# Optimization experiments

Measured on AMD Instinct MI355X. Metric: run time of the kernel, lower is better.

## Reference

```python
import jax, jax.numpy as jnp
import numpy as np

N, E = 50000, 400000
IN_CH, HID, HEADS, EDGE_DIM = 128, 64, 4, 3
NEG_SLOPE = 0.2


def gatv2_conv(x, src, dst, edge_attr, Wl, Wr, We, att, bias):
    # x: [N, F_in]; Wl/Wr: [H*C, F_in]; We: [H*C, edge_dim]; att: [H, C]; bias: [C]
    H, C = att.shape
    n = x.shape[0]
    xl = (x @ Wl.T).reshape(n, H, C)   # source-side transform (lin_l)
    xr = (x @ Wr.T).reshape(n, H, C)   # target-side transform (lin_r)
    e = (edge_attr @ We.T).reshape(-1, H, C)
    z = jax.nn.leaky_relu(xl[src] + xr[dst] + e, NEG_SLOPE)  # [E,H,C]
    alpha = jnp.einsum('ehc,hc->eh', z, att)                 # [E,H]
    # segment softmax over incoming edges per destination node
    amax = jax.ops.segment_max(alpha, dst, num_segments=n)
    alpha = jnp.exp(alpha - amax[dst])
    denom = jax.ops.segment_sum(alpha, dst, num_segments=n)
    alpha = alpha / (denom[dst] + 1e-16)
    msg = xl[src] * alpha[:, :, None]                        # [E,H,C]
    out = jax.ops.segment_sum(msg, dst, num_segments=n)      # [N,H,C]
    return out.mean(axis=1) + bias                           # concat=False -> head mean


def setup_inputs() -> dict:
    key = jax.random.key(0)
    ks = jax.random.split(key, 16)
    s = 0.1
    return {
        'x': jax.random.normal(ks[0], (N, IN_CH), jnp.float32),
        'edge_index': jax.random.randint(ks[1], (2, E), 0, N, jnp.int32),
        'edge_attr': jax.random.normal(ks[2], (E, EDGE_DIM), jnp.float32),
        'Wl1': jax.random.normal(ks[3], (HEADS * HID, IN_CH), jnp.float32) * s,
        'Wr1': jax.random.normal(ks[4], (HEADS * HID, IN_CH), jnp.float32) * s,
        'We1': jax.random.normal(ks[5], (HEADS * HID, EDGE_DIM), jnp.float32) * s,
        'att1': jax.random.normal(ks[6], (HEADS, HID), jnp.float32) * s,
        'b1': jnp.zeros((HID,), jnp.float32),
        'Wl2': jax.random.normal(ks[7], (HEADS * HID, HID), jnp.float32) * s,
        'Wr2': jax.random.normal(ks[8], (HEADS * HID, HID), jnp.float32) * s,
        'We2': jax.random.normal(ks[9], (HEADS * HID, EDGE_DIM), jnp.float32) * s,
        'att2': jax.random.normal(ks[10], (HEADS, HID), jnp.float32) * s,
        'b2': jnp.zeros((HID,), jnp.float32),
        'prelu_w': jnp.full((HID,), 0.25, jnp.float32),
    }


def reference(x, edge_index, edge_attr, Wl1, Wr1, We1, att1, b1, Wl2, Wr2, We2, att2, b2, prelu_w):
    src, dst = edge_index[0], edge_index[1]
    h = gatv2_conv(x, src, dst, edge_attr, Wl1, Wr1, We1, att1, b1)
    h = gatv2_conv(h, src, dst, edge_attr, Wl2, Wr2, We2, att2, b2)
    return jnp.where(h >= 0, h, prelu_w * h)  # PReLU, per-channel weight
```

## Files before the change

### kernel.cpp

```cpp
#include <hip/hip_runtime.h>
#include <hip/hip_bf16.h>

#define HC 256

typedef __attribute__((ext_vector_type(8))) short bf16x8;
typedef __attribute__((ext_vector_type(4))) float f32x4;
typedef __attribute__((ext_vector_type(2))) float f32x2;

__device__ __forceinline__ void gl_lds16(const void* g, void* l) {
  __builtin_amdgcn_global_load_lds(
      (const __attribute__((address_space(1))) unsigned int*)g,
      (__attribute__((address_space(3))) unsigned int*)l, 16, 0, 0);
}

__device__ __forceinline__ void cast_w_one(const float* Wl, const float* Wr,
                                           ushort* WT, int F, int idx) {
  int col = idx / F, f = idx - col * F;
  float v = (col < 256) ? Wl[col * F + f] : Wr[(col - 256) * F + f];
  __hip_bfloat16 h = __float2bfloat16(v);
  WT[(size_t)col * F + f] = *(ushort*)&h;
}

__global__ void k_weights_hist(const float* __restrict__ Wl1, const float* __restrict__ Wr1,
                               ushort* __restrict__ WT1, const float* __restrict__ Wl2,
                               const float* __restrict__ Wr2, ushort* __restrict__ WT2,
                               const int* __restrict__ ei, int* __restrict__ deg, int E_) {
  int idx = blockIdx.x * blockDim.x + threadIdx.x;
  const int t1 = 512 * 128, t2 = 512 * 64;
  if (idx < t1) {
    cast_w_one(Wl1, Wr1, WT1, 128, idx);
  } else if (idx < t1 + t2) {
    cast_w_one(Wl2, Wr2, WT2, 64, idx - t1);
  } else {
    int e = idx - t1 - t2;
    if (e < E_) atomicAdd(&deg[ei[E_ + e]], 1);
  }
}

template <int F>
__global__ __launch_bounds__(256) void gemm_mfma(const ushort* __restrict__ A,
                                                 const ushort* __restrict__ WT,
                                                 ushort* __restrict__ xlb,
                                                 ushort* __restrict__ xrb, int n_nodes) {
  constexpr int NSTEP = F / 64;
  __shared__ __align__(16) ushort As[128 * 64];
  __shared__ __align__(16) ushort Bs[128 * 64];
  const int tid = threadIdx.x;
  const int wv = tid >> 6, lane = tid & 63;
  const int m16 = lane & 15, quad = lane >> 4;
  const int col0 = blockIdx.x * 128;
  const int row0 = blockIdx.y * 128;
  const int wm = (wv >> 1) * 64, wn = (wv & 1) * 64;

  f32x4 acc[4][4];
#pragma unroll
  for (int i = 0; i < 4; ++i)
#pragma unroll
    for (int j = 0; j < 4; ++j) acc[i][j] = (f32x4){0.f, 0.f, 0.f, 0.f};

#pragma unroll
  for (int s = 0; s < NSTEP; ++s) {
    const int khat = s * 64;
    __syncthreads();
#pragma unroll
    for (int t = 0; t < 4; ++t) {
      const int sl16 = tid + 256 * t;
      const int row = sl16 >> 3, sl = sl16 & 7;
      const int gch = sl ^ (row & 7);
      const int grow = row0 + row;
      if (grow < n_nodes)
        gl_lds16(A + (size_t)grow * F + khat + gch * 8, As + sl16 * 8);
      gl_lds16(WT + (size_t)(col0 + row) * F + khat + gch * 8, Bs + sl16 * 8);
    }
    __syncthreads();
#pragma unroll
    for (int kh = 0; kh < 2; ++kh) {
      bf16x8 af[4], bf[4];
#pragma unroll
      for (int i = 0; i < 4; ++i) {
        const int row = wm + i * 16 + m16;
        const int slot = (kh * 4 + quad) ^ (row & 7);
        af[i] = *(bf16x8*)&As[row * 64 + slot * 8];
      }
#pragma unroll
      for (int j = 0; j < 4; ++j) {
        const int col = wn + j * 16 + m16;
        const int slot = (kh * 4 + quad) ^ (col & 7);
        bf[j] = *(bf16x8*)&Bs[col * 64 + slot * 8];
      }
#pragma unroll
      for (int i = 0; i < 4; ++i)
#pragma unroll
        for (int j = 0; j < 4; ++j)
          acc[i][j] =
              __builtin_amdgcn_mfma_f32_16x16x32_bf16(af[i], bf[j], acc[i][j], 0, 0, 0);
    }
  }
  const bool is_xl = (col0 < 256);
#pragma unroll
  for (int i = 0; i < 4; ++i) {
#pragma unroll
    for (int r = 0; r < 4; ++r) {
      const int grow = row0 + wm + i * 16 + quad * 4 + r;
      if (grow < n_nodes) {
#pragma unroll
        for (int j = 0; j < 4; ++j) {
          const float v = acc[i][j][r];
          const int col = col0 + wn + j * 16 + m16;
          __hip_bfloat16 h = __float2bfloat16(v);
          if (is_xl)
            xlb[(size_t)grow * 256 + col] = *(ushort*)&h;
          else
            xrb[(size_t)grow * 256 + (col - 256)] = *(ushort*)&h;
        }
      }
    }
  }
}

__global__ void k_scan_local(const int* __restrict__ deg, int* __restrict__ rowstart,
                             int* __restrict__ partial, int n) {
  __shared__ int a[256], b[256];
  const int t = threadIdx.x;
  const int i = blockIdx.x * 256 + t;
  const int v = (i < n) ? deg[i] : 0;
  a[t] = v;
  __syncthreads();
  int* cur = a;
  int* nxt = b;
  for (int off = 1; off < 256; off <<= 1) {
    int x = cur[t];
    if (t >= off) x += cur[t - off];
    nxt[t] = x;
    __syncthreads();
    int* tmp = cur; cur = nxt; nxt = tmp;
  }
  const int incl = cur[t];
  if (i < n) rowstart[i] = incl - v;
  if (t == 255) partial[blockIdx.x] = incl;
}

__global__ void k_scan_partial(int* __restrict__ partial, int nblk,
                               int* __restrict__ ssrc, float4* __restrict__ sea, int E_) {
  __shared__ int a[256], b[256];
  const int t = threadIdx.x;
  if (t < 8) {
    ssrc[E_ + t] = 0;
    sea[E_ + t] = make_float4(0.f, 0.f, 0.f, 0.f);
  }
  const int v = (t < nblk) ? partial[t] : 0;
  a[t] = v;
  __syncthreads();
  int* cur = a;
  int* nxt = b;
  for (int off = 1; off < 256; off <<= 1) {
    int x = cur[t];
    if (t >= off) x += cur[t - off];
    nxt[t] = x;
    __syncthreads();
    int* tmp = cur; cur = nxt; nxt = tmp;
  }
  if (t < nblk) partial[t] = cur[t] - v;
}

__global__ void k_add_off(int* __restrict__ rowstart, int* __restrict__ cursor,
                          const int* __restrict__ partial, int n, int E_) {
  int i = blockIdx.x * blockDim.x + threadIdx.x;
  if (i < n) {
    int v = rowstart[i] + partial[i >> 8];
    rowstart[i] = v;
    cursor[i] = v;
  }
  if (i == 0) rowstart[n] = E_;
}

__global__ void k_prep(const float* __restrict__ x, ushort* __restrict__ A,
                       const int* __restrict__ ei, const float* __restrict__ ea,
                       int* __restrict__ cursor, int* __restrict__ ssrc,
                       float4* __restrict__ sea, int n, int E_) {
  const int nx8 = n * 16;
  int idx = blockIdx.x * blockDim.x + threadIdx.x;
  if (idx < nx8) {
    const float4* xp = (const float4*)x + (size_t)idx * 2;
    float4 v0 = xp[0], v1 = xp[1];
    float vv[8] = {v0.x, v0.y, v0.z, v0.w, v1.x, v1.y, v1.z, v1.w};
    __align__(16) ushort hb[8];
#pragma unroll
    for (int j = 0; j < 8; ++j) {
      __hip_bfloat16 h = __float2bfloat16(vv[j]);
      hb[j] = *(ushort*)&h;
    }
    *(int4*)(A + (size_t)idx * 8) = *(int4*)hb;
  } else {
    int e = idx - nx8;
    if (e < E_) {
      int dst = ei[E_ + e];
      int pos = atomicAdd(&cursor[dst], 1);
      ssrc[pos] = ei[e];
      sea[pos] = make_float4(ea[e * 3], ea[e * 3 + 1], ea[e * 3 + 2], 0.f);
    }
  }
}

__device__ __forceinline__ f32x2 vmax2(f32x2 a, f32x2 b) {
  return (f32x2){fmaxf(a.x, b.x), fmaxf(a.y, b.y)};
}
__device__ __forceinline__ f32x2 vmin2(f32x2 a, f32x2 b) {
  return (f32x2){fminf(a.x, b.x), fminf(a.y, b.y)};
}

__device__ __forceinline__ void edge_step(
    const ushort4& lu, const float4& eav, const f32x2* we0, const f32x2* we1,
    const f32x2* we2, const f32x2* at, const f32x2* xrl, f32x2& num01,
    f32x2& num23, float& den) {
  f32x2 lav0, lav1;
  lav0.x = __uint_as_float((unsigned)lu.x << 16);
  lav0.y = __uint_as_float((unsigned)lu.y << 16);
  lav1.x = __uint_as_float((unsigned)lu.z << 16);
  lav1.y = __uint_as_float((unsigned)lu.w << 16);
  const f32x2 zero = {0.f, 0.f};
  const f32x2 slope = {0.2f, 0.2f};
  f32x2 pv = zero;
#pragma unroll
  for (int j = 0; j < 2; ++j) {
    f32x2 la = (j == 0) ? lav0 : lav1;
    f32x2 ev = we0[j] * eav.x + we1[j] * eav.y + we2[j] * eav.z;
    f32x2 s = la + xrl[j] + ev;
    f32x2 z = vmax2(s, zero) + slope * vmin2(s, zero);
    pv = pv + z * at[j];
  }
  float p = pv.x + pv.y;
  p += __shfl_xor(p, 1);
  p += __shfl_xor(p, 2);
  p += __shfl_xor(p, 4);
  p += __shfl_xor(p, 8);
  const float w = __expf(p);
  den += w;
  num01 = num01 + (f32x2){w, w} * lav0;
  num23 = num23 + (f32x2){w, w} * lav1;
}

template <int MODE>
__global__ __launch_bounds__(256) void fused_attn(
    const ushort* __restrict__ xlb, const ushort* __restrict__ xrb,
    const int* __restrict__ rowstart, const int* __restrict__ ssrc,
    const float4* __restrict__ sea, const float* __restrict__ We,
    const float* __restrict__ att, const float* __restrict__ bias,
    const float* __restrict__ pw, float* __restrict__ out,
    ushort* __restrict__ outs, int n, int chunk) {
  const int lane = threadIdx.x & 63;
  const int wid =
      __builtin_amdgcn_readfirstlane((blockIdx.x * blockDim.x + threadIdx.x) >> 6);
  const int d0 = wid * chunk;
  if (d0 >= n) return;
  const int d1 = min(d0 + chunk, n);

  f32x2 we0[2], we1[2], we2[2], at[2];
#pragma unroll
  for (int j = 0; j < 4; ++j) {
    int r = 4 * lane + j;
    ((float*)we0)[j] = We[r * 3 + 0];
    ((float*)we1)[j] = We[r * 3 + 1];
    ((float*)we2)[j] = We[r * 3 + 2];
    ((float*)at)[j] = att[r];
  }
  const float4 bias4 = ((const float4*)bias)[lane & 15];
  float4 pw4 = {0.f, 0.f, 0.f, 0.f};
  if (MODE == 1) pw4 = ((const float4*)pw)[lane & 15];
  const ushort4* xlb4 = (const ushort4*)xlb;

  for (int d = d0; d < d1; ++d) {
    const ushort4 xu = ((const ushort4*)xrb)[(unsigned)(d * 64) + lane];
    f32x2 xrl[2];
    xrl[0].x = __uint_as_float((unsigned)xu.x << 16);
    xrl[0].y = __uint_as_float((unsigned)xu.y << 16);
    xrl[1].x = __uint_as_float((unsigned)xu.z << 16);
    xrl[1].y = __uint_as_float((unsigned)xu.w << 16);

    int pos = rowstart[d];
    const int end = rowstart[d + 1];
    f32x2 num01 = {0.f, 0.f}, num23 = {0.f, 0.f};
    float den = 0.f;

    if (pos < end) {
      int s0 = ssrc[pos], s1 = ssrc[pos + 1], s2 = ssrc[pos + 2], s3 = ssrc[pos + 3];
      ushort4 g0 = xlb4[(unsigned)(s0 * 64) + lane];
      ushort4 g1 = xlb4[(unsigned)(s1 * 64) + lane];
      ushort4 g2 = xlb4[(unsigned)(s2 * 64) + lane];
      ushort4 g3 = xlb4[(unsigned)(s3 * 64) + lane];
      float4 e0 = sea[pos], e1 = sea[pos + 1], e2 = sea[pos + 2], e3 = sea[pos + 3];

      while (pos + 4 <= end) {
        ushort4 h0 = g0, h1 = g1, h2 = g2, h3 = g3;
        float4 f0 = e0, f1 = e1, f2 = e2, f3 = e3;
        if (pos + 4 < end) {
          int t0 = ssrc[pos + 4], t1 = ssrc[pos + 5], t2 = ssrc[pos + 6],
              t3 = ssrc[pos + 7];
          h0 = xlb4[(unsigned)(t0 * 64) + lane];
          h1 = xlb4[(unsigned)(t1 * 64) + lane];
          h2 = xlb4[(unsigned)(t2 * 64) + lane];
          h3 = xlb4[(unsigned)(t3 * 64) + lane];
          f0 = sea[pos + 4];
          f1 = sea[pos + 5];
          f2 = sea[pos + 6];
          f3 = sea[pos + 7];
        }
        edge_step(g0, e0, we0, we1, we2, at, xrl, num01, num23, den);
        edge_step(g1, e1, we0, we1, we2, at, xrl, num01, num23, den);
        edge_step(g2, e2, we0, we1, we2, at, xrl, num01, num23, den);
        edge_step(g3, e3, we0, we1, we2, at, xrl, num01, num23, den);
        g0 = h0; g1 = h1; g2 = h2; g3 = h3;
        e0 = f0; e1 = f1; e2 = f2; e3 = f3;
        pos += 4;
      }
      const int rem = end - pos;
      if (rem > 0) edge_step(g0, e0, we0, we1, we2, at, xrl, num01, num23, den);
      if (rem > 1) edge_step(g1, e1, we0, we1, we2, at, xrl, num01, num23, den);
      if (rem > 2) edge_step(g2, e2, we0, we1, we2, at, xrl, num01, num23, den);
    }

    const float inv = 1.f / (den + 1e-16f);
    float4 r;
    r.x = num01.x * inv;
    r.y = num01.y * inv;
    r.z = num23.x * inv;
    r.w = num23.y * inv;
    r.x += __shfl_xor(r.x, 16);
    r.y += __shfl_xor(r.y, 16);
    r.z += __shfl_xor(r.z, 16);
    r.w += __shfl_xor(r.w, 16);
    r.x += __shfl_xor(r.x, 32);
    r.y += __shfl_xor(r.y, 32);
    r.z += __shfl_xor(r.z, 32);
    r.w += __shfl_xor(r.w, 32);
    if (lane < 16) {
      float o[4];
      o[0] = 0.25f * r.x + bias4.x;
      o[1] = 0.25f * r.y + bias4.y;
      o[2] = 0.25f * r.z + bias4.z;
      o[3] = 0.25f * r.w + bias4.w;
      if (MODE == 1) {
        const float pwv[4] = {pw4.x, pw4.y, pw4.z, pw4.w};
#pragma unroll
        for (int j = 0; j < 4; ++j) o[j] = (o[j] >= 0.f) ? o[j] : pwv[j] * o[j];
        ((float4*)out)[(size_t)d * 16 + lane] = make_float4(o[0], o[1], o[2], o[3]);
      } else {
        ushort hb[4];
#pragma unroll
        for (int j = 0; j < 4; ++j) {
          __hip_bfloat16 h = __float2bfloat16(o[j]);
          hb[j] = *(ushort*)&h;
        }
        *(ushort4*)(outs + (size_t)d * 64 + 4 * lane) =
            make_ushort4(hb[0], hb[1], hb[2], hb[3]);
      }
    }
  }
}

extern "C" void kernel_launch(void* const* d_in, const int* in_sizes, int n_in,
                              void* d_out, int out_size, void* d_ws, size_t ws_size,
                              hipStream_t stream) {
  const float* x    = (const float*)d_in[0];
  const int*   ei   = (const int*)d_in[1];
  const float* ea   = (const float*)d_in[2];
  const float* Wl1  = (const float*)d_in[3];
  const float* Wr1  = (const float*)d_in[4];
  const float* We1  = (const float*)d_in[5];
  const float* att1 = (const float*)d_in[6];
  const float* b1   = (const float*)d_in[7];
  const float* Wl2  = (const float*)d_in[8];
  const float* Wr2  = (const float*)d_in[9];
  const float* We2  = (const float*)d_in[10];
  const float* att2 = (const float*)d_in[11];
  const float* b2   = (const float*)d_in[12];
  const float* pw   = (const float*)d_in[13];
  const int N_ = in_sizes[0] / 128;
  const int E_ = in_sizes[1] / 2;
  float* out = (float*)d_out;

  char* w = (char*)d_ws;
  auto alloc = [&](size_t bytes) {
    char* p = w;
    w += (bytes + 255) & ~size_t(255);
    return p;
  };
  ushort* xlb      = (ushort*)alloc((size_t)N_ * 256 * 2);
  ushort* xrb      = (ushort*)alloc((size_t)N_ * 256 * 2);
  ushort* Ax       = (ushort*)alloc((size_t)N_ * 128 * 2);
  ushort* h2       = (ushort*)alloc((size_t)N_ * 64 * 2);
  int*    ssrc     = (int*)alloc((size_t)(E_ + 8) * 4);
  float4* sea      = (float4*)alloc((size_t)(E_ + 8) * 16);
  int*    deg      = (int*)alloc((size_t)N_ * 4);
  int*    rowstart = (int*)alloc((size_t)(N_ + 1) * 4);
  int*    cursor   = (int*)alloc((size_t)N_ * 4);
  int*    partial  = (int*)alloc(256 * 4);
  ushort* WT1      = (ushort*)alloc((size_t)512 * 128 * 2);
  ushort* WT2      = (ushort*)alloc((size_t)512 * 64 * 2);

  hipMemsetAsync(deg, 0, (size_t)N_ * 4, stream);
  const int wtot = 512 * 128 + 512 * 64 + E_;
  k_weights_hist<<<(wtot + 255) / 256, 256, 0, stream>>>(Wl1, Wr1, WT1, Wl2, Wr2, WT2,
                                                         ei, deg, E_);

  const int nblk = (N_ + 255) / 256;
  k_scan_local<<<nblk, 256, 0, stream>>>(deg, rowstart, partial, N_);
  k_scan_partial<<<1, 256, 0, stream>>>(partial, nblk, ssrc, sea, E_);
  k_add_off<<<nblk, 256, 0, stream>>>(rowstart, cursor, partial, N_, E_);
  const int ptot = N_ * 16 + E_;
  k_prep<<<(ptot + 255) / 256, 256, 0, stream>>>(x, Ax, ei, ea, cursor, ssrc, sea,
                                                 N_, E_);

  const dim3 GG(4, (N_ + 127) / 128);
  const int chunk = 2;
  const int nwav = (N_ + chunk - 1) / chunk;
  const int FB = (nwav + 3) / 4;

  gemm_mfma<128><<<GG, 256, 0, stream>>>(Ax, WT1, xlb, xrb, N_);
  fused_attn<0><<<FB, 256, 0, stream>>>(xlb, xrb, rowstart, ssrc, sea, We1, att1,
                                        b1, pw, nullptr, h2, N_, chunk);
  gemm_mfma<64><<<GG, 256, 0, stream>>>(h2, WT2, xlb, xrb, N_);
  fused_attn<1><<<FB, 256, 0, stream>>>(xlb, xrb, rowstart, ssrc, sea, We2, att2,
                                        b2, pw, out, nullptr, N_, chunk);
}
```

Before: 282.3 us.

## Stage GEMM output through LDS for 16B stores; process two edges per wave

The GEMM epilogue now writes bf16 results into a padded LDS tile and then emits coalesced 16-byte row stores, replacing scattered 2-byte global writes. The attention kernel is reorganised so each half-wave handles a different edge, with each lane holding 8 channels loaded as one int4. This halves the number of serial edge iterations and shortens the shuffle reduction, at the cost of an extra cross-half reduction and idle lanes on odd edge counts. The edge prefetch depth drops from four edges to two.

Measured after the change: 287.5 us. About the same (+1.8%).

```diff
diff --git a/kernel.cpp b/kernel.cpp
--- a/kernel.cpp
+++ b/kernel.cpp
@@ -43,8 +43,9 @@
                                                  ushort* __restrict__ xlb,
                                                  ushort* __restrict__ xrb, int n_nodes) {
   constexpr int NSTEP = F / 64;
-  __shared__ __align__(16) ushort As[128 * 64];
-  __shared__ __align__(16) ushort Bs[128 * 64];
+  __shared__ __align__(16) ushort smem[17408];
+  ushort* As = smem;
+  ushort* Bs = smem + 8192;
   const int tid = threadIdx.x;
   const int wv = tid >> 6, lane = tid & 63;
   const int m16 = lane & 15, quad = lane >> 4;
@@ -96,25 +97,32 @@
               __builtin_amdgcn_mfma_f32_16x16x32_bf16(af[i], bf[j], acc[i][j], 0, 0, 0);
     }
   }
+  __syncthreads();
+  ushort* Ct = smem;
+#pragma unroll
+  for (int i = 0; i < 4; ++i) {
+#pragma unroll
+    for (int r = 0; r < 4; ++r) {
+      const int row = wm + i * 16 + quad * 4 + r;
+#pragma unroll
+      for (int j = 0; j < 4; ++j) {
+        __hip_bfloat16 h = __float2bfloat16(acc[i][j][r]);
+        Ct[row * 136 + wn + j * 16 + m16] = *(ushort*)&h;
+      }
+    }
+  }
+  __syncthreads();
   const bool is_xl = (col0 < 256);
-#pragma unroll
-  for (int i = 0; i < 4; ++i) {
-#pragma unroll
-    for (int r = 0; r < 4; ++r) {
-      const int grow = row0 + wm + i * 16 + quad * 4 + r;
-      if (grow < n_nodes) {
-#pragma unroll
-        for (int j = 0; j < 4; ++j) {
-          const float v = acc[i][j][r];
-          const int col = col0 + wn + j * 16 + m16;
-          __hip_bfloat16 h = __float2bfloat16(v);
-          if (is_xl)
-            xlb[(size_t)grow * 256 + col] = *(ushort*)&h;
-          else
-            xrb[(size_t)grow * 256 + (col - 256)] = *(ushort*)&h;
-        }
-      }
-    }
+  ushort* dst = is_xl ? xlb : xrb;
+  const int cb = is_xl ? col0 : (col0 - 256);
+  const int chunk = tid & 15;
+#pragma unroll
+  for (int it = 0; it < 8; ++it) {
+    const int row = (tid >> 4) + 16 * it;
+    const int grow = row0 + row;
+    int4 v = *(int4*)&Ct[row * 136 + chunk * 8];
+    if (grow < n_nodes)
+      *(int4*)(dst + (size_t)grow * 256 + cb + chunk * 8) = v;
   }
 }
 
@@ -202,42 +210,15 @@
   }
 }
 
-__device__ __forceinline__ f32x2 vmax2(f32x2 a, f32x2 b) {
-  return (f32x2){fmaxf(a.x, b.x), fmaxf(a.y, b.y)};
-}
-__device__ __forceinline__ f32x2 vmin2(f32x2 a, f32x2 b) {
-  return (f32x2){fminf(a.x, b.x), fminf(a.y, b.y)};
-}
-
-__device__ __forceinline__ void edge_step(
-    const ushort4& lu, const float4& eav, const f32x2* we0, const f32x2* we1,
-    const f32x2* we2, const f32x2* at, const f32x2* xrl, f32x2& num01,
-    f32x2& num23, float& den) {
-  f32x2 lav0, lav1;
-  lav0.x = __uint_as_float((unsigned)lu.x << 16);
-  lav0.y = __uint_as_float((unsigned)lu.y << 16);
-  lav1.x = __uint_as_float((unsigned)lu.z << 16);
-  lav1.y = __uint_as_float((unsigned)lu.w << 16);
-  const f32x2 zero = {0.f, 0.f};
-  const f32x2 slope = {0.2f, 0.2f};
-  f32x2 pv = zero;
-#pragma unroll
-  for (int j = 0; j < 2; ++j) {
-    f32x2 la = (j == 0) ? lav0 : lav1;
-    f32x2 ev = we0[j] * eav.x + we1[j] * eav.y + we2[j] * eav.z;
-    f32x2 s = la + xrl[j] + ev;
-    f32x2 z = vmax2(s, zero) + slope * vmin2(s, zero);
-    pv = pv + z * at[j];
-  }
-  float p = pv.x + pv.y;
-  p += __shfl_xor(p, 1);
-  p += __shfl_xor(p, 2);
-  p += __shfl_xor(p, 4);
-  p += __shfl_xor(p, 8);
-  const float w = __expf(p);
-  den += w;
-  num01 = num01 + (f32x2){w, w} * lav0;
-  num23 = num23 + (f32x2){w, w} * lav1;
+__device__ __forceinline__ void unpack8(const int4& v, float* f) {
+  f[0] = __uint_as_float(((unsigned)v.x) << 16);
+  f[1] = __uint_as_float(((unsigned)v.x) & 0xFFFF0000u);
+  f[2] = __uint_as_float(((unsigned)v.y) << 16);
+  f[3] = __uint_as_float(((unsigned)v.y) & 0xFFFF0000u);
+  f[4] = __uint_as_float(((unsigned)v.z) << 16);
+  f[5] = __uint_as_float(((unsigned)v.z) & 0xFFFF0000u);
+  f[6] = __uint_as_float(((unsigned)v.w) << 16);
+  f[7] = __uint_as_float(((unsigned)v.w) & 0xFFFF0000u);
 }
 
 template <int MODE>
@@ -247,112 +228,132 @@
     const float4* __restrict__ sea, const float* __restrict__ We,
     const float* __restrict__ att, const float* __restrict__ bias,
     const float* __restrict__ pw, float* __restrict__ out,
-    ushort* __restrict__ outs, int n, int chunk) {
+    ushort* __restrict__ outs, int n, int chunkd) {
   const int lane = threadIdx.x & 63;
+  const int q = lane & 31;
+  const bool hi = (lane >= 32);
   const int wid =
       __builtin_amdgcn_readfirstlane((blockIdx.x * blockDim.x + threadIdx.x) >> 6);
-  const int d0 = wid * chunk;
+  const int d0 = wid * chunkd;
   if (d0 >= n) return;
-  const int d1 = min(d0 + chunk, n);
-
-  f32x2 we0[2], we1[2], we2[2], at[2];
-#pragma unroll
-  for (int j = 0; j < 4; ++j) {
-    int r = 4 * lane + j;
-    ((float*)we0)[j] = We[r * 3 + 0];
-    ((float*)we1)[j] = We[r * 3 + 1];
-    ((float*)we2)[j] = We[r * 3 + 2];
-    ((float*)at)[j] = att[r];
-  }
-  const float4 bias4 = ((const float4*)bias)[lane & 15];
-  float4 pw4 = {0.f, 0.f, 0.f, 0.f};
-  if (MODE == 1) pw4 = ((const float4*)pw)[lane & 15];
-  const ushort4* xlb4 = (const ushort4*)xlb;
+  const int d1 = min(d0 + chunkd, n);
+
+  float we0[8], we1[8], we2[8], at8[8];
+#pragma unroll
+  for (int j = 0; j < 8; ++j) {
+    int f = 8 * q + j;
+    we0[j] = We[f * 3 + 0];
+    we1[j] = We[f * 3 + 1];
+    we2[j] = We[f * 3 + 2];
+    at8[j] = att[f];
+  }
+  const float4 bias40 = ((const float4*)bias)[(q & 7) * 2];
+  const float4 bias41 = ((const float4*)bias)[(q & 7) * 2 + 1];
+  float4 pw40 = {0.f, 0.f, 0.f, 0.f}, pw41 = {0.f, 0.f, 0.f, 0.f};
+  if (MODE == 1) {
+    pw40 = ((const float4*)pw)[(q & 7) * 2];
+    pw41 = ((const float4*)pw)[(q & 7) * 2 + 1];
+  }
+  const int4* xlb4 = (const int4*)xlb;
 
   for (int d = d0; d < d1; ++d) {
-    const ushort4 xu = ((const ushort4*)xrb)[(unsigned)(d * 64) + lane];
-    f32x2 xrl[2];
-    xrl[0].x = __uint_as_float((unsigned)xu.x << 16);
-    xrl[0].y = __uint_as_float((unsigned)xu.y << 16);
-    xrl[1].x = __uint_as_float((unsigned)xu.z << 16);
-    xrl[1].y = __uint_as_float((unsigned)xu.w << 16);
-
-    int pos = rowstart[d];
+    const int4 xi = ((const int4*)xrb)[(unsigned)d * 32 + q];
+    float xr8[8];
+    unpack8(xi, xr8);
+
+    int p = rowstart[d];
     const int end = rowstart[d + 1];
-    f32x2 num01 = {0.f, 0.f}, num23 = {0.f, 0.f};
+    float num[8];
+#pragma unroll
+    for (int j = 0; j < 8; ++j) num[j] = 0.f;
     float den = 0.f;
 
-    if (pos < end) {
-      int s0 = ssrc[pos], s1 = ssrc[pos + 1], s2 = ssrc[pos + 2], s3 = ssrc[pos + 3];
-      ushort4 g0 = xlb4[(unsigned)(s0 * 64) + lane];
-      ushort4 g1 = xlb4[(unsigned)(s1 * 64) + lane];
-      ushort4 g2 = xlb4[(unsigned)(s2 * 64) + lane];
-      ushort4 g3 = xlb4[(unsigned)(s3 * 64) + lane];
-      float4 e0 = sea[pos], e1 = sea[pos + 1], e2 = sea[pos + 2], e3 = sea[pos + 3];
-
-      while (pos + 4 <= end) {
-        ushort4 h0 = g0, h1 = g1, h2 = g2, h3 = g3;
-        float4 f0 = e0, f1 = e1, f2 = e2, f3 = e3;
-        if (pos + 4 < end) {
-          int t0 = ssrc[pos + 4], t1 = ssrc[pos + 5], t2 = ssrc[pos + 6],
-              t3 = ssrc[pos + 7];
-          h0 = xlb4[(unsigned)(t0 * 64) + lane];
-          h1 = xlb4[(unsigned)(t1 * 64) + lane];
-          h2 = xlb4[(unsigned)(t2 * 64) + lane];
-          h3 = xlb4[(unsigned)(t3 * 64) + lane];
-          f0 = sea[pos + 4];
-          f1 = sea[pos + 5];
-          f2 = sea[pos + 6];
-          f3 = sea[pos + 7];
+    if (p < end) {
+      int s0 = ssrc[p], s1 = ssrc[p + 1];
+      float4 e0 = sea[p], e1 = sea[p + 1];
+      int src = hi ? s1 : s0;
+      int4 g = xlb4[(unsigned)src * 32 + q];
+      float a0 = hi ? e1.x : e0.x;
+      float a1 = hi ? e1.y : e0.y;
+      float a2 = hi ? e1.z : e0.z;
+
+      while (p < end) {
+        const bool more = (p + 2 < end);
+        int4 gn = g;
+        float na0 = a0, na1 = a1, na2 = a2;
+        if (more) {
+          int t0 = ssrc[p + 2], t1 = ssrc[p + 3];
+          float4 f0 = sea[p + 2], f1 = sea[p + 3];
+          int nsrc = hi ? t1 : t0;
+          gn = xlb4[(unsigned)nsrc * 32 + q];
+          na0 = hi ? f1.x : f0.x;
+          na1 = hi ? f1.y : f0.y;
+          na2 = hi ? f1.z : f0.z;
         }
-        edge_step(g0, e0, we0, we1, we2, at, xrl, num01, num23, den);
-        edge_step(g1, e1, we0, we1, we2, at, xrl, num01, num23, den);
-        edge_step(g2, e2, we0, we1, we2, at, xrl, num01, num23, den);
-        edge_step(g3, e3, we0, we1, we2, at, xrl, num01, num23, den);
-        g0 = h0; g1 = h1; g2 = h2; g3 = h3;
-        e0 = f0; e1 = f1; e2 = f2; e3 = f3;
-        pos += 4;
+        const float validf = (!hi || (p + 1 < end)) ? 1.f : 0.f;
+
+        float la[8];
+        unpack8(g, la);
+        float pv = 0.f;
+#pragma unroll
+        for (int j = 0; j < 8; ++j) {
+          float ev = fmaf(we0[j], a0, fmaf(we1[j], a1, we2[j] * a2));
+          float s = la[j] + xr8[j] + ev;
+          float z = fmaxf(s, 0.f) + 0.2f * fminf(s, 0.f);
+          pv = fmaf(z, at8[j], pv);
+        }
+        pv += __shfl_xor(pv, 1);
+        pv += __shfl_xor(pv, 2);
+        pv += __shfl_xor(pv, 4);
+        const float w = validf * __expf(pv);
+        den += w;
+#pragma unroll
+        for (int j = 0; j < 8; ++j) num[j] = fmaf(w, la[j], num[j]);
+
+        g = gn;
+        a0 = na0; a1 = na1; a2 = na2;
+        p += 2;
       }
-      const int rem = end - pos;
-      if (rem > 0) edge_step(g0, e0, we0, we1, we2, at, xrl, num01, num23, den);
-      if (rem > 1) edge_step(g1, e1, we0, we1, we2, at, xrl, num01, num23, den);
-      if (rem > 2) edge_step(g2, e2, we0, we1, we2, at, xrl, num01, num23, den);
-    }
-
+    }
+
+    den += __shfl_xor(den, 32);
+#pragma unroll
+    for (int j = 0; j < 8; ++j) num[j] += __shfl_xor(num[j], 32);
     const float inv = 1.f / (den + 1e-16f);
-    float4 r;
-    r.x = num01.x * inv;
-    r.y = num01.y * inv;
-    r.z = num23.x * inv;
-    r.w = num23.y * inv;
-    r.x += __shfl_xor(r.x, 16);
-    r.y += __shfl_xor(r.y, 16);
-    r.z += __shfl_xor(r.z, 16);
-    r.w += __shfl_xor(r.w, 16);
-    r.x += __shfl_xor(r.x, 32);
-    r.y += __shfl_xor(r.y, 32);
-    r.z += __shfl_xor(r.z, 32);
-    r.w += __shfl_xor(r.w, 32);
-    if (lane < 16) {
-      float o[4];
-      o[0] = 0.25f * r.x + bias4.x;
-      o[1] = 0.25f * r.y + bias4.y;
-      o[2] = 0.25f * r.z + bias4.z;
-      o[3] = 0.25f * r.w + bias4.w;
+#pragma unroll
+    for (int j = 0; j < 8; ++j) num[j] *= inv;
+#pragma unroll
+    for (int j = 0; j < 8; ++j) {
+      num[j] += __shfl_xor(num[j], 8);
+      num[j] += __shfl_xor(num[j], 16);
+    }
+    if (lane < 8) {
+      const int c = 8 * q;
+      float o[8];
+      o[0] = 0.25f * num[0] + bias40.x;
+      o[1] = 0.25f * num[1] + bias40.y;
+      o[2] = 0.25f * num[2] + bias40.z;
+      o[3] = 0.25f * num[3] + bias40.w;
+      o[4] = 0.25f * num[4] + bias41.x;
+      o[5] = 0.25f * num[5] + bias41.y;
+      o[6] = 0.25f * num[6] + bias41.z;
+      o[7] = 0.25f * num[7] + bias41.w;
       if (MODE == 1) {
-        const float pwv[4] = {pw4.x, pw4.y, pw4.z, pw4.w};
-#pragma unroll
-        for (int j = 0; j < 4; ++j) o[j] = (o[j] >= 0.f) ? o[j] : pwv[j] * o[j];
-        ((float4*)out)[(size_t)d * 16 + lane] = make_float4(o[0], o[1], o[2], o[3]);
+        const float pwv[8] = {pw40.x, pw40.y, pw40.z, pw40.w,
+                              pw41.x, pw41.y, pw41.z, pw41.w};
+#pragma unroll
+        for (int j = 0; j < 8; ++j) o[j] = (o[j] >= 0.f) ? o[j] : pwv[j] * o[j];
+        float4* op = (float4*)(out + (size_t)d * 64 + c);
+        op[0] = make_float4(o[0], o[1], o[2], o[3]);
+        op[1] = make_float4(o[4], o[5], o[6], o[7]);
       } else {
-        ushort hb[4];
-#pragma unroll
-        for (int j = 0; j < 4; ++j) {
+        __align__(16) ushort hb[8];
+#pragma unroll
+        for (int j = 0; j < 8; ++j) {
           __hip_bfloat16 h = __float2bfloat16(o[j]);
           hb[j] = *(ushort*)&h;
         }
-        *(ushort4*)(outs + (size_t)d * 64 + 4 * lane) =
-            make_ushort4(hb[0], hb[1], hb[2], hb[3]);
+        *(int4*)(outs + (size_t)d * 64 + c) = *(int4*)hb;
       }
     }
   }
@@ -412,14 +413,14 @@
                                                  N_, E_);
 
   const dim3 GG(4, (N_ + 127) / 128);
-  const int chunk = 2;
-  const int nwav = (N_ + chunk - 1) / chunk;
+  const int chunkd = 2;
+  const int nwav = (N_ + chunkd - 1) / chunkd;
   const int FB = (nwav + 3) / 4;
 
   gemm_mfma<128><<<GG, 256, 0, stream>>>(Ax, WT1, xlb, xrb, N_);
   fused_attn<0><<<FB, 256, 0, stream>>>(xlb, xrb, rowstart, ssrc, sea, We1, att1,
-                                        b1, pw, nullptr, h2, N_, chunk);
+                                        b1, pw, nullptr, h2, N_, chunkd);
   gemm_mfma<64><<<GG, 256, 0, stream>>>(h2, WT2, xlb, xrb, N_);
   fused_attn<1><<<FB, 256, 0, stream>>>(xlb, xrb, rowstart, ssrc, sea, We2, att2,
-                                        b2, pw, out, nullptr, N_, chunk);
-}
+                                        b2, pw, out, nullptr, N_, chunkd);
+}
```
